# Kernel optimization log

Hardware: AMD Instinct MI355X
Metric: run time of the kernel (lower is better)

Reference implementation:

```python
import jax, jax.numpy as jnp
import numpy as np

B, TMAX, N = 8192, 2048, 2  # batch, max sequence length, hidden states


def setup_inputs() -> dict:
    key = jax.random.key(0)
    k1, k2 = jax.random.split(key)
    x = jax.random.randint(k1, (B, TMAX), 0, 2, dtype=jnp.int32)          # binary observations
    T = jax.random.randint(k2, (B, 1), 1, TMAX + 1, dtype=jnp.int32)     # valid lengths in [1, TMAX]
    combined_input = jnp.concatenate([x, T], axis=1)                      # (B, TMAX+1)
    # learned parameters (initial values hardcoded in the torch module)
    state_prior_logits = jnp.array([0.3, 0.7], dtype=jnp.float32)
    transition_logits = jnp.array([[0.9, 0.1], [0.85, 0.15]], dtype=jnp.float32)
    emission_logits = jnp.array([[0.8, 0.2], [0.6, 0.4]], dtype=jnp.float32)
    return {
        "combined_input": combined_input,
        "state_prior_logits": state_prior_logits,
        "transition_logits": transition_logits,
        "emission_logits": emission_logits,
    }


def reference(combined_input, state_prior_logits, transition_logits, emission_logits):
    x = combined_input[:, :-1]          # (B, TMAX) int observations
    T = combined_input[:, -1]           # (B,) lengths
    priors = jax.nn.softmax(state_prior_logits)                 # (N,)
    A = jax.nn.softmax(transition_logits, axis=1)               # (N, N)
    emT = jax.nn.softmax(emission_logits, axis=1).T             # (M, N): emT[obs] == emission_probs[:, obs]

    alpha0 = emT[x[:, 0]] * priors                              # (B, N)

    def step(alpha, xt):
        # alpha_t[:, n] = p(obs_t | n) * sum_m alpha_{t-1}[:, m] * A[m, n]
        alpha = emT[xt] * (alpha @ A)
        return alpha, alpha.sum(axis=-1)

    _, sums = jax.lax.scan(step, alpha0, x[:, 1:].T)            # sums: (TMAX-1, B)
    probs = jnp.concatenate([alpha0.sum(axis=-1)[None, :], sums], axis=0).T  # (B, TMAX)
    final_probs = jnp.take_along_axis(probs, (T - 1)[:, None], axis=1)       # (B, 1)
    return final_probs
```

## Files before the change

### kernel.cpp

```cpp
#include <hip/hip_runtime.h>

#define TMAX_C 2048
#define ROWLEN (TMAX_C + 1)

__global__ __launch_bounds__(256, 8) void hmm_fwd_kernel(
    const int* __restrict__ combined,
    const float* __restrict__ sp,
    const float* __restrict__ tr,
    const float* __restrict__ emi,
    float* __restrict__ out, int B)
{
    const int lane = threadIdx.x & 63;
    const int wave_in_block = threadIdx.x >> 6;
    const int b = blockIdx.x * (blockDim.x >> 6) + wave_in_block;
    if (b >= B) return;

    float p0 = __expf(sp[0]), p1 = __expf(sp[1]);
    { float s = p0 + p1; p0 /= s; p1 /= s; }

    float A00, A01, A10, A11;
    { float e0 = __expf(tr[0]), e1 = __expf(tr[1]); float s = e0 + e1; A00 = e0/s; A01 = e1/s; }
    { float e0 = __expf(tr[2]), e1 = __expf(tr[3]); float s = e0 + e1; A10 = e0/s; A11 = e1/s; }

    float em00, em01, em10, em11;
    { float e0 = __expf(emi[0]), e1 = __expf(emi[1]); float s = e0 + e1; em00 = e0/s; em01 = e1/s; }
    { float e0 = __expf(emi[2]), e1 = __expf(emi[3]); float s = e0 + e1; em10 = e0/s; em11 = e1/s; }

    const float M0_00 = A00*em00, M0_01 = A01*em10, M0_10 = A10*em00, M0_11 = A11*em10;
    const float M1_00 = A00*em01, M1_01 = A01*em11, M1_10 = A10*em01, M1_11 = A11*em11;

    const int* __restrict__ row = combined + (size_t)b * ROWLEN;
    const int T = row[TMAX_C];
    const int steps = T - 1;
    const int chunk = (steps + 63) >> 6;

    float P00 = 1.f, P01 = 0.f, P10 = 0.f, P11 = 1.f;
    const int start = 1 + lane * chunk;
    const int end   = min(start + chunk, T);
    for (int t = start; t < end; ++t) {
        const int xt = row[t];
        const float m00 = xt ? M1_00 : M0_00;
        const float m01 = xt ? M1_01 : M0_01;
        const float m10 = xt ? M1_10 : M0_10;
        const float m11 = xt ? M1_11 : M0_11;
        const float n00 = P00*m00 + P01*m10;
        const float n01 = P00*m01 + P01*m11;
        const float n10 = P10*m00 + P11*m10;
        const float n11 = P10*m01 + P11*m11;
        P00 = n00; P01 = n01; P10 = n10; P11 = n11;
    }

    #pragma unroll
    for (int off = 1; off < 64; off <<= 1) {
        const float q00 = __shfl_down(P00, off);
        const float q01 = __shfl_down(P01, off);
        const float q10 = __shfl_down(P10, off);
        const float q11 = __shfl_down(P11, off);
        if (lane + off < 64) {
            const float n00 = P00*q00 + P01*q10;
            const float n01 = P00*q01 + P01*q11;
            const float n10 = P10*q00 + P11*q10;
            const float n11 = P10*q01 + P11*q11;
            P00 = n00; P01 = n01; P10 = n10; P11 = n11;
        }
    }

    if (lane == 0) {
        const int x0 = row[0];
        const float a0 = (x0 ? em01 : em00) * p0;
        const float a1 = (x0 ? em11 : em10) * p1;
        const float v0 = a0*P00 + a1*P10;
        const float v1 = a0*P01 + a1*P11;
        out[b] = v0 + v1;
    }
}

extern "C" void kernel_launch(void* const* d_in, const int* in_sizes, int n_in,
                              void* d_out, int out_size, void* d_ws, size_t ws_size,
                              hipStream_t stream) {
    const int*   combined = (const int*)d_in[0];
    const float* sp       = (const float*)d_in[1];
    const float* tr       = (const float*)d_in[2];
    const float* emi      = (const float*)d_in[3];
    float* out = (float*)d_out;

    const int B = out_size;
    const int waves_per_block = 4;
    const int grid = (B + waves_per_block - 1) / waves_per_block;
    hmm_fwd_kernel<<<grid, 256, 0, stream>>>(combined, sp, tr, emi, out, B);
}
```

Baseline: 119.9 us.

## Load observations coalesced and bit-pack via ballot before fixed 32-step scan

Replaces the per-lane strided reads of each lane's time chunk with lane-contiguous loads of 64-step words, and packs the binary observations into 64-bit masks with __ballot. Each lane then takes 32 bits of one mask and runs a fully unrolled 32-step matrix product, predicated on the valid step count. This targets uncoalesced global loads and the data-dependent serial loop. In exchange every lane always runs 32 predicated steps, and each wave issues up to 32 loads per lane regardless of sequence length.

```diff
diff --git a/kernel.cpp b/kernel.cpp
--- a/kernel.cpp
+++ b/kernel.cpp
@@ -11,8 +11,7 @@
     float* __restrict__ out, int B)
 {
     const int lane = threadIdx.x & 63;
-    const int wave_in_block = threadIdx.x >> 6;
-    const int b = blockIdx.x * (blockDim.x >> 6) + wave_in_block;
+    const int b = blockIdx.x * (blockDim.x >> 6) + (threadIdx.x >> 6);
     if (b >= B) return;
 
     float p0 = __expf(sp[0]), p1 = __expf(sp[1]);
@@ -32,22 +31,46 @@
     const int* __restrict__ row = combined + (size_t)b * ROWLEN;
     const int T = row[TMAX_C];
     const int steps = T - 1;
-    const int chunk = (steps + 63) >> 6;
+    const int nwords = (steps + 63) >> 6;
+    const int my_word = lane >> 1;
+
+    unsigned long long my_mask = 0ULL;
+    #pragma unroll
+    for (int g = 0; g < 4; ++g) {
+        if ((g << 3) < nwords) {
+            int a[8];
+            #pragma unroll
+            for (int u = 0; u < 8; ++u) {
+                a[u] = row[1 + (((g << 3) + u) << 6) + lane];
+            }
+            #pragma unroll
+            for (int u = 0; u < 8; ++u) {
+                const unsigned long long m = __ballot(a[u] != 0);
+                if (((g << 3) + u) == my_word) my_mask = m;
+            }
+        }
+    }
+    const unsigned int bits = (lane & 1) ? (unsigned int)(my_mask >> 32)
+                                         : (unsigned int)my_mask;
+    const int cnt = min(max(steps - (lane << 5), 0), 32);
 
     float P00 = 1.f, P01 = 0.f, P10 = 0.f, P11 = 1.f;
-    const int start = 1 + lane * chunk;
-    const int end   = min(start + chunk, T);
-    for (int t = start; t < end; ++t) {
-        const int xt = row[t];
-        const float m00 = xt ? M1_00 : M0_00;
-        const float m01 = xt ? M1_01 : M0_01;
-        const float m10 = xt ? M1_10 : M0_10;
-        const float m11 = xt ? M1_11 : M0_11;
+    #pragma unroll
+    for (int j = 0; j < 32; ++j) {
+        const bool bit = (bits >> j) & 1u;
+        const float m00 = bit ? M1_00 : M0_00;
+        const float m01 = bit ? M1_01 : M0_01;
+        const float m10 = bit ? M1_10 : M0_10;
+        const float m11 = bit ? M1_11 : M0_11;
         const float n00 = P00*m00 + P01*m10;
         const float n01 = P00*m01 + P01*m11;
         const float n10 = P10*m00 + P11*m10;
         const float n11 = P10*m01 + P11*m11;
-        P00 = n00; P01 = n01; P10 = n10; P11 = n11;
+        const bool ok = j < cnt;
+        P00 = ok ? n00 : P00;
+        P01 = ok ? n01 : P01;
+        P10 = ok ? n10 : P10;
+        P11 = ok ? n11 : P11;
     }
 
     #pragma unroll
```

New measurement: 102.8 us. 1.17x faster.
